# Kernel optimization log

Measured on AMD Instinct MI355X. Metric: run time of the kernel, lower is better.

Reference implementation:

```python
import jax, jax.numpy as jnp
import numpy as np

B, S, DM, H, D = 4, 2048, 1024, 16, 64
CAP = 15.0
EPS = 1e-6


def setup_inputs() -> dict:
    key = jax.random.key(0)
    ks = jax.random.split(key, 5)
    return {
        "x": jax.random.normal(ks[0], (B, S, DM), jnp.float32),
        "hidden_state": jnp.zeros((B, H, D, D), jnp.float32),
        "w_qkv": jax.random.normal(ks[1], (3 * H * D, DM), jnp.float32) * 0.02,
        "w_gate": jax.random.normal(ks[2], (3 * H, DM), jnp.float32) * 0.02,
        "w_out": jax.random.normal(ks[3], (DM, H * D), jnp.float32) * 0.02,
        "ln_w": jnp.ones((DM,), jnp.float32),
    }


def reference(x, hidden_state, w_qkv, w_gate, w_out, ln_w):
    Bq, Sq, DMq = x.shape
    residual = x
    # RMSNorm (computed in float32, matching the torch module)
    xf = x.astype(jnp.float32)
    var = jnp.mean(xf * xf, axis=-1, keepdims=True)
    xn = ln_w * (xf * jax.lax.rsqrt(var + EPS)).astype(x.dtype)
    # Fused qkv projection: (B,S,3,H,D)
    qkv = jnp.einsum('bsd,od->bso', xn, w_qkv).reshape(Bq, Sq, 3, H, D)
    q, k, v = qkv[:, :, 0], qkv[:, :, 1], qkv[:, :, 2]
    # Gates: (B,S,3,H) -> soft cap -> sigmoid
    gates = jnp.einsum('bsd,od->bso', xn, w_gate).reshape(Bq, Sq, 3, H)
    gates = jax.nn.sigmoid(CAP * jnp.tanh(gates / CAP))
    ig, fg, og = gates[:, :, 0], gates[:, :, 1], gates[:, :, 2]

    def step(h, inp):
        q_t, k_t, v_t, i_t, f_t, o_t = inp  # q/k/v: (B,H,D); gates: (B,H)
        kv = jnp.einsum('bhd,bhe->bhde', k_t, v_t)
        h = f_t[..., None, None] * h + i_t[..., None, None] * kv
        out = o_t[..., None] * jnp.einsum('bhd,bhde->bhe', q_t, h)
        return h, out

    xs = (q.swapaxes(0, 1), k.swapaxes(0, 1), v.swapaxes(0, 1),
          ig.swapaxes(0, 1), fg.swapaxes(0, 1), og.swapaxes(0, 1))
    h_final, outs = jax.lax.scan(step, hidden_state, xs)  # outs: (S,B,H,D)
    output = outs.swapaxes(0, 1).reshape(Bq, Sq, H * D)
    y = residual + output @ w_out.T
    return y, h_final
```

## Files before the change

kernel.cpp:

```cpp
#include <hip/hip_runtime.h>
#include <hip/hip_bf16.h>
#include <math.h>
#include <stdint.h>

#define Bq 4
#define Sq 2048
#define DMq 1024
#define Hq 16
#define Dq 64
#define CAPf 15.0f
#define EPSf 1e-6f
#define Tc 64
#define Cc (Sq / Tc)
#define QKVW (3 * Hq * Dq)
#define NGATE (3 * Hq)
#define NPAD 3200
#define MSc (Bq * Sq)

typedef __attribute__((ext_vector_type(8))) short short8;
typedef __attribute__((ext_vector_type(4))) float f32x4;
typedef __hip_bfloat16 bf16;

__device__ __forceinline__ float b2f(bf16 v) { return __bfloat162float(v); }
__device__ __forceinline__ bf16  f2b(float v) { return __float2bfloat16(v); }
__device__ __forceinline__ uint16_t f2bu(float f) {
    bf16 h = __float2bfloat16(f); uint16_t u; __builtin_memcpy(&u, &h, 2); return u;
}
__device__ __forceinline__ float bu2f(uint16_t u) {
    uint32_t x = ((uint32_t)u) << 16; float f; __builtin_memcpy(&f, &x, 4); return f;
}
__device__ __forceinline__ float gate_act(float v) {
    float t = v * (1.0f / CAPf);
    float e2 = __expf(2.0f * t);
    float th = 1.0f - 2.0f / (e2 + 1.0f);
    return 1.0f / (1.0f + __expf(-CAPf * th));
}

__global__ void prep_kernel(const float* __restrict__ x,
                            const float* __restrict__ ln_w,
                            const float* __restrict__ wqkv,
                            const float* __restrict__ wgate,
                            const float* __restrict__ wout,
                            bf16* __restrict__ xn,
                            bf16* __restrict__ wcomb, bf16* __restrict__ wob) {
    int tid = threadIdx.x;
    if (blockIdx.x < MSc) {
        int row = blockIdx.x;
        const float4* xr = (const float4*)(x + (size_t)row * DMq);
        float4 v = xr[tid];
        float ss = v.x*v.x + v.y*v.y + v.z*v.z + v.w*v.w;
        #pragma unroll
        for (int off = 32; off > 0; off >>= 1) ss += __shfl_down(ss, off);
        __shared__ float red[4];
        int lane = tid & 63, wv = tid >> 6;
        if (lane == 0) red[wv] = ss;
        __syncthreads();
        float tot = red[0] + red[1] + red[2] + red[3];
        float rs = rsqrtf(tot * (1.0f / DMq) + EPSf);
        float4 w4 = ((const float4*)ln_w)[tid];
        bf16 t[4] = {f2b(v.x * rs * w4.x), f2b(v.y * rs * w4.y),
                     f2b(v.z * rs * w4.z), f2b(v.w * rs * w4.w)};
        *(uint2*)(xn + (size_t)row * DMq + tid * 4) = *(uint2*)t;
        return;
    }
    const int n1 = QKVW * DMq / 4;
    const int n2 = (NPAD - QKVW) * DMq / 4;
    const int ng = NGATE * DMq / 4;
    const int n3 = DMq * Hq * Dq / 4;
    int i = (blockIdx.x - MSc) * 256 + tid;
    if (i < n1) {
        float4 v = ((const float4*)wqkv)[i];
        bf16 t[4] = {f2b(v.x), f2b(v.y), f2b(v.z), f2b(v.w)};
        ((uint2*)wcomb)[i] = *(uint2*)t;
    } else if (i < n1 + n2) {
        int j = i - n1;
        uint2 o = make_uint2(0u, 0u);
        if (j < ng) {
            float4 v = ((const float4*)wgate)[j];
            bf16 t[4] = {f2b(v.x), f2b(v.y), f2b(v.z), f2b(v.w)};
            o = *(uint2*)t;
        }
        ((uint2*)wcomb)[n1 + j] = o;
    } else if (i < n1 + n2 + n3) {
        int j = i - n1 - n2;
        float4 v = ((const float4*)wout)[j];
        bf16 t[4] = {f2b(v.x), f2b(v.y), f2b(v.z), f2b(v.w)};
        ((uint2*)wob)[j] = *(uint2*)t;
    }
}

enum Epi { EPI_BF16 = 0, EPI_GATE = 1, EPI_RESID = 2 };

template<int EPI>
__global__ __launch_bounds__(256) void gemm_mfma(const bf16* __restrict__ A,
                                                 const bf16* __restrict__ Bw,
                                                 const float* __restrict__ resid,
                                                 void* __restrict__ Cv,
                                                 int M, int N, int K) {
    __shared__ bf16 As[128 * 64];
    __shared__ bf16 Bs[128 * 64];
    const int tid = threadIdx.x;
    const int w = tid >> 6;
    const int l = tid & 63;
    const int wr = (w >> 1) * 64;
    const int wc = (w & 1) * 64;
    const int bm = blockIdx.y * 128;
    const int bn = blockIdx.x * 128;

    const int lrow = l >> 3;
    const int swzc = ((l & 7) ^ lrow) * 8;

    const int fl = l & 15;
    const int kb = l >> 4;
    const int rsw = l & 7;

    f32x4 acc[4][4];
    #pragma unroll
    for (int i = 0; i < 4; i++)
        #pragma unroll
        for (int j = 0; j < 4; j++) acc[i][j] = (f32x4){0.f, 0.f, 0.f, 0.f};

    for (int k0 = 0; k0 < K; k0 += 64) {
        __syncthreads();
        #pragma unroll
        for (int inst = 0; inst < 4; inst++) {
            int r0 = w * 32 + inst * 8;
            const bf16* gp = A + (size_t)(bm + r0 + lrow) * K + k0 + swzc;
            __builtin_amdgcn_global_load_lds(
                (const __attribute__((address_space(1))) uint32_t*)gp,
                (__attribute__((address_space(3))) uint32_t*)(As + r0 * 64),
                16, 0, 0);
        }
        #pragma unroll
        for (int inst = 0; inst < 4; inst++) {
            int r0 = w * 32 + inst * 8;
            if (bn + r0 < N) {
                const bf16* gp = Bw + (size_t)(bn + r0 + lrow) * K + k0 + swzc;
                __builtin_amdgcn_global_load_lds(
                    (const __attribute__((address_space(1))) uint32_t*)gp,
                    (__attribute__((address_space(3))) uint32_t*)(Bs + r0 * 64),
                    16, 0, 0);
            }
        }
        __syncthreads();
        #pragma unroll
        for (int kk2 = 0; kk2 < 2; kk2++) {
            const int koff = (((kk2 << 2) + kb) ^ rsw) * 8;
            short8 af[4], bfr[4];
            #pragma unroll
            for (int i = 0; i < 4; i++)
                af[i] = *(const short8*)(As + (wr + i * 16 + fl) * 64 + koff);
            #pragma unroll
            for (int j = 0; j < 4; j++)
                bfr[j] = *(const short8*)(Bs + (wc + j * 16 + fl) * 64 + koff);
            #pragma unroll
            for (int i = 0; i < 4; i++)
                #pragma unroll
                for (int j = 0; j < 4; j++)
                    acc[i][j] = __builtin_amdgcn_mfma_f32_16x16x32_bf16(
                        af[i], bfr[j], acc[i][j], 0, 0, 0);
        }
    }

    #pragma unroll
    for (int i = 0; i < 4; i++) {
        #pragma unroll
        for (int j = 0; j < 4; j++) {
            int col = bn + wc + j * 16 + fl;
            if (EPI == EPI_GATE && col >= N) continue;
            #pragma unroll
            for (int r = 0; r < 4; r++) {
                int row = bm + wr + i * 16 + kb * 4 + r;
                size_t idx = (size_t)row * N + col;
                float v = acc[i][j][r];
                if (EPI == EPI_GATE) {
                    ((float*)Cv)[idx] = gate_act(v);
                } else if (EPI == EPI_RESID) {
                    ((float*)Cv)[idx] = v + resid[idx];
                } else {
                    ((bf16*)Cv)[idx] = f2b(v);
                }
            }
        }
    }
}
template __global__ void gemm_mfma<EPI_BF16>(const bf16*, const bf16*, const float*, void*, int, int, int);
template __global__ void gemm_mfma<EPI_GATE>(const bf16*, const bf16*, const float*, void*, int, int, int);
template __global__ void gemm_mfma<EPI_RESID>(const bf16*, const bf16*, const float*, void*, int, int, int);

__global__ __launch_bounds__(64) void gemm_gates(const bf16* __restrict__ A,
                                                 const bf16* __restrict__ Bw,
                                                 float* __restrict__ gates_t,
                                                 int M, int K) {
    const int bm = blockIdx.x * 32;
    const int l = threadIdx.x, fl = l & 15, kb = l >> 4;
    f32x4 acc[2][3];
    #pragma unroll
    for (int i = 0; i < 2; i++)
        #pragma unroll
        for (int j = 0; j < 3; j++) acc[i][j] = (f32x4){0.f, 0.f, 0.f, 0.f};

    for (int ks = 0; ks < K; ks += 32) {
        short8 af[2], bf[3];
        #pragma unroll
        for (int i = 0; i < 2; i++)
            af[i] = *(const short8*)(A + (size_t)(bm + i * 16 + fl) * K + ks + kb * 8);
        #pragma unroll
        for (int j = 0; j < 3; j++)
            bf[j] = *(const short8*)(Bw + (size_t)(j * 16 + fl) * K + ks + kb * 8);
        #pragma unroll
        for (int i = 0; i < 2; i++)
            #pragma unroll
            for (int j = 0; j < 3; j++)
                acc[i][j] = __builtin_amdgcn_mfma_f32_16x16x32_bf16(af[i], bf[j], acc[i][j], 0, 0, 0);
    }
    #pragma unroll
    for (int i = 0; i < 2; i++)
        #pragma unroll
        for (int j = 0; j < 3; j++)
            #pragma unroll
            for (int r = 0; r < 4; r++) {
                int row = bm + i * 16 + kb * 4 + r;
                int g = j * 16 + fl;
                gates_t[(size_t)g * M + row] = gate_act(acc[i][j][r]);
            }
}

__global__ __launch_bounds__(64) void chunk_intra(const bf16* __restrict__ qkvb,
                                                  const float* __restrict__ gates,
                                                  bf16* __restrict__ attb,
                                                  bf16* __restrict__ LT,
                                                  float* __restrict__ oaArr,
                                                  float* __restrict__ Fch) {
    const int blk = blockIdx.x;
    const int c  = blk & (Cc - 1);
    const int bh = blk >> 5;
    const int b = bh >> 4, hh = bh & 15;
    const int l = threadIdx.x;
    const int s0 = c * Tc;

    __shared__ bf16 KTs[4096];
    __shared__ bf16 VTs[4096];
    __shared__ float rowS[64], pcolS[64], wstS[64];

    const int rix = b * Sq + s0 + l;
    float ig = gates[(size_t)(0 * Hq + hh) * MSc + rix];
    float fg = gates[(size_t)(1 * Hq + hh) * MSc + rix];
    float og = gates[(size_t)(2 * Hq + hh) * MSc + rix];
    float la = __logf(fg);
    #pragma unroll
    for (int off = 1; off < 64; off <<= 1) {
        float v = __shfl_up(la, off);
        if (l >= off) la += v;
    }
    float la63 = __shfl(la, 63);
    float li = __logf(ig);
    rowS[l]  = la + __logf(og);
    pcolS[l] = li - la;
    wstS[l]  = __expf(la63 - la + li);
    float oa = og * __expf(la);
    oaArr[(size_t)blk * 64 + l] = oa;
    if (l == 0) Fch[blk] = __expf(la63);
    __syncthreads();

    const int cg = l & 7, rp = l >> 3;
    const size_t rowBase = (size_t)(b * Sq + s0);
    const int kcol = (Hq + hh) * Dq, vcol = (2 * Hq + hh) * Dq;
    #pragma unroll
    for (int pass = 0; pass < 4; pass++) {
        int j0 = pass * 16 + rp * 2;
        const bf16* r0 = qkvb + (rowBase + j0) * QKVW;
        const bf16* r1 = qkvb + (rowBase + j0 + 1) * QKVW;
        short8 k0 = *(const short8*)(r0 + kcol + cg * 8);
        short8 k1 = *(const short8*)(r1 + kcol + cg * 8);
        short8 v0 = *(const short8*)(r0 + vcol + cg * 8);
        short8 v1 = *(const short8*)(r1 + vcol + cg * 8);
        float w0 = wstS[j0], w1 = wstS[j0 + 1];
        #pragma unroll
        for (int s = 0; s < 8; s++) {
            int cc = cg * 8 + s;
            int base = cc * 64 + ((((j0 >> 3) ^ (cc & 7) ^ (cc >> 3))) << 3) + (j0 & 7);
            uint32_t kp = (uint32_t)f2bu(bu2f((uint16_t)k0[s]) * w0)
                        | ((uint32_t)f2bu(bu2f((uint16_t)k1[s]) * w1) << 16);
            uint32_t vp = (uint32_t)(uint16_t)v0[s] | ((uint32_t)(uint16_t)v1[s] << 16);
            *(uint32_t*)&KTs[base] = kp;
            *(uint32_t*)&VTs[base] = vp;
        }
    }
    __syncthreads();

    const int fl = l & 15, kb = l >> 4;

    f32x4 accL[4][4];
    #pragma unroll
    for (int i = 0; i < 4; i++)
        #pragma unroll
        for (int j = 0; j < 4; j++) accL[i][j] = (f32x4){0.f, 0.f, 0.f, 0.f};
    #pragma unroll
    for (int ks = 0; ks < 2; ks++) {
        short8 vt[4], kt[4];
        #pragma unroll
        for (int i = 0; i < 4; i++) {
            int row = i * 16 + fl;
            int koff = (((ks * 4 + kb) ^ (row & 7) ^ (row >> 3))) << 3;
            vt[i] = *(const short8*)(VTs + row * 64 + koff);
            kt[i] = *(const short8*)(KTs + row * 64 + koff);
        }
        #pragma unroll
        for (int i = 0; i < 4; i++)
            #pragma unroll
            for (int j = 0; j < 4; j++)
                accL[i][j] = __builtin_amdgcn_mfma_f32_16x16x32_bf16(vt[i], kt[j], accL[i][j], 0, 0, 0);
    }
    #pragma unroll
    for (int i = 0; i < 4; i++)
        #pragma unroll
        for (int j = 0; j < 4; j++)
            #pragma unroll
            for (int r = 0; r < 4; r++) {
                int rr = i * 16 + kb * 4 + r, cc2 = j * 16 + fl;
                LT[(size_t)blk * 4096 + rr * 64 + cc2] = f2b(accL[i][j][r]);
            }

    const bf16* Qb = qkvb + rowBase * QKVW + hh * Dq;
    const bf16* Kb = qkvb + rowBase * QKVW + kcol;
    f32x4 accS[4][4];
    #pragma unroll
    for (int i = 0; i < 4; i++)
        #pragma unroll
        for (int j = 0; j < 4; j++) accS[i][j] = (f32x4){0.f, 0.f, 0.f, 0.f};
    #pragma unroll
    for (int ks = 0; ks < 2; ks++) {
        short8 qf[4], kf[4];
        #pragma unroll
        for (int i = 0; i < 4; i++)
            qf[i] = *(const short8*)(Qb + (size_t)(i * 16 + fl) * QKVW + ks * 32 + kb * 8);
        #pragma unroll
        for (int j = 0; j < 4; j++)
            kf[j] = *(const short8*)(Kb + (size_t)(j * 16 + fl) * QKVW + ks * 32 + kb * 8);
        #pragma unroll
        for (int i = 0; i < 4; i++)
            #pragma unroll
            for (int j = 0; j < 4; j++)
                accS[i][j] = __builtin_amdgcn_mfma_f32_16x16x32_bf16(qf[i], kf[j], accS[i][j], 0, 0, 0);
    }

    __syncthreads();
    bf16* Ps = KTs;
    #pragma unroll
    for (int i = 0; i < 4; i++) {
        #pragma unroll
        for (int j = 0; j < 4; j++) {
            int jj = j * 16 + fl;
            float pc = pcolS[jj];
            #pragma unroll
            for (int r = 0; r < 4; r++) {
                int t = i * 16 + kb * 4 + r;
                float p = (jj <= t) ? __expf(rowS[t] + pc) * accS[i][j][r] : 0.f;
                int slot = (jj >> 3) ^ (t & 7) ^ (t >> 3);
                Ps[t * 64 + slot * 8 + (jj & 7)] = f2b(p);
            }
        }
    }
    __syncthreads();

    f32x4 accO[4][4];
    #pragma unroll
    for (int i = 0; i < 4; i++)
        #pragma unroll
        for (int j = 0; j < 4; j++) accO[i][j] = (f32x4){0.f, 0.f, 0.f, 0.f};
    #pragma unroll
    for (int ks = 0; ks < 2; ks++) {
        short8 pf[4], vt[4];
        #pragma unroll
        for (int i = 0; i < 4; i++) {
            int row = i * 16 + fl;
            int koff = (((ks * 4 + kb) ^ (row & 7) ^ (row >> 3))) << 3;
            pf[i] = *(const short8*)(Ps  + row * 64 + koff);
            vt[i] = *(const short8*)(VTs + row * 64 + koff);
        }
        #pragma unroll
        for (int i = 0; i < 4; i++)
            #pragma unroll
            for (int j = 0; j < 4; j++)
                accO[i][j] = __builtin_amdgcn_mfma_f32_16x16x32_bf16(pf[i], vt[j], accO[i][j], 0, 0, 0);
    }

    #pragma unroll
    for (int i = 0; i < 4; i++)
        #pragma unroll
        for (int j = 0; j < 4; j++)
            #pragma unroll
            for (int r = 0; r < 4; r++) {
                int rr = i * 16 + kb * 4 + r, cc2 = j * 16 + fl;
                attb[(rowBase + rr) * (Hq * Dq) + hh * Dq + cc2] = f2b(accO[i][j][r]);
            }
}

__global__ __launch_bounds__(256) void scan_pass2(bf16* __restrict__ LH,
                                                  const float* __restrict__ Fchunk,
                                                  const float* __restrict__ h0,
                                                  float* __restrict__ hfin) {
    int idx = blockIdx.x * 256 + threadIdx.x;
    int bh = idx >> 12;
    int ed = idx & 4095;
    int e = ed >> 6, d = ed & 63;
    float run = h0[(size_t)bh * 4096 + d * 64 + e];
    #pragma unroll
    for (int c = 0; c < Cc; c++) {
        float Fv = Fchunk[bh * Cc + c];
        size_t off = ((size_t)bh * Cc + c) * 4096 + ed;
        float Lv = b2f(LH[off]);
        LH[off] = f2b(run);
        run = Fv * run + Lv;
    }
    hfin[(size_t)bh * 4096 + d * 64 + e] = run;
}

__global__ __launch_bounds__(64) void chunk_cross(const bf16* __restrict__ qkvb,
                                                  const bf16* __restrict__ HT,
                                                  const float* __restrict__ oaArr,
                                                  bf16* __restrict__ attb) {
    const int blk = blockIdx.x;
    const int c = blk & (Cc - 1);
    const int bh = blk >> 5;
    const int b = bh >> 4, hh = bh & 15;
    const int l = threadIdx.x, fl = l & 15, kb = l >> 4;
    const size_t rowBase = (size_t)(b * Sq + c * Tc);
    __shared__ float oaS[64];
    oaS[l] = oaArr[(size_t)blk * 64 + l];
    __syncthreads();
    const bf16* Qb = qkvb + rowBase * QKVW + hh * Dq;
    const bf16* Hb = HT + (size_t)blk * 4096;
    f32x4 acc[4][4];
    #pragma unroll
    for (int i = 0; i < 4; i++)
        #pragma unroll
        for (int j = 0; j < 4; j++) acc[i][j] = (f32x4){0.f, 0.f, 0.f, 0.f};
    #pragma unroll
    for (int ks = 0; ks < 2; ks++) {
        short8 qf[4], hf[4];
        #pragma unroll
        for (int i = 0; i < 4; i++)
            qf[i] = *(const short8*)(Qb + (size_t)(i * 16 + fl) * QKVW + ks * 32 + kb * 8);
        #pragma unroll
        for (int j = 0; j < 4; j++)
            hf[j] = *(const short8*)(Hb + (j * 16 + fl) * 64 + ks * 32 + kb * 8);
        #pragma unroll
        for (int i = 0; i < 4; i++)
            #pragma unroll
            for (int j = 0; j < 4; j++)
                acc[i][j] = __builtin_amdgcn_mfma_f32_16x16x32_bf16(qf[i], hf[j], acc[i][j], 0, 0, 0);
    }
    #pragma unroll
    for (int i = 0; i < 4; i++)
        #pragma unroll
        for (int j = 0; j < 4; j++)
            #pragma unroll
            for (int r = 0; r < 4; r++) {
                int t = i * 16 + kb * 4 + r, e = j * 16 + fl;
                size_t idx = (rowBase + t) * (Hq * Dq) + hh * Dq + e;
                attb[idx] = f2b(b2f(attb[idx]) + oaS[t] * acc[i][j][r]);
            }
}

extern "C" void kernel_launch(void* const* d_in, const int* in_sizes, int n_in,
                              void* d_out, int out_size, void* d_ws, size_t ws_size,
                              hipStream_t stream) {
    const float* x      = (const float*)d_in[0];
    const float* h0     = (const float*)d_in[1];
    const float* w_qkv  = (const float*)d_in[2];
    const float* w_gate = (const float*)d_in[3];
    const float* w_out  = (const float*)d_in[4];
    const float* ln_w   = (const float*)d_in[5];

    const size_t MS = (size_t)Bq * Sq;
    const size_t BH = (size_t)Bq * Hq;

    float* p = (float*)d_ws;
    bf16*  xnb   = (bf16*)p;  p += MS * DMq / 2;
    bf16*  qkvb  = (bf16*)p;  p += MS * QKVW / 2;
    float* gates = p;         p += MS * NGATE;
    float* oaArr = p;         p += BH * Cc * Tc;
    float* Fch   = p;         p += BH * Cc;
    bf16*  LT    = (bf16*)p;  p += BH * Cc * Dq * Dq / 2;
    bf16*  wcomb = (bf16*)p;  p += (size_t)NPAD * DMq / 2;
    bf16*  wob   = (bf16*)p;  p += (size_t)DMq * Hq * Dq / 2;
    size_t need = (size_t)(p - (float*)d_ws) * sizeof(float);
    if (ws_size < need) return;
    bf16* attb = xnb;

    float* y    = (float*)d_out;
    float* hfin = y + MS * DMq;

    const int cvt_n = (QKVW * DMq + (NPAD - QKVW) * DMq + DMq * Hq * Dq) / 4;
    const int cvt_blocks = (cvt_n + 255) / 256;
    prep_kernel<<<dim3(MS + cvt_blocks), dim3(256), 0, stream>>>(
        x, ln_w, w_qkv, w_gate, w_out, xnb, wcomb, wob);

    gemm_mfma<EPI_BF16><<<dim3(QKVW / 128, MS / 128), dim3(256), 0, stream>>>(
        xnb, wcomb, nullptr, qkvb, (int)MS, QKVW, DMq);

    gemm_gates<<<dim3(MS / 32), dim3(64), 0, stream>>>(
        xnb, wcomb + (size_t)QKVW * DMq, gates, (int)MS, DMq);

    chunk_intra<<<dim3(BH * Cc), dim3(64), 0, stream>>>(qkvb, gates, attb, LT, oaArr, Fch);
    scan_pass2<<<dim3(BH * 4096 / 256), dim3(256), 0, stream>>>(LT, Fch, h0, hfin);
    chunk_cross<<<dim3(BH * Cc), dim3(64), 0, stream>>>(qkvb, LT, oaArr, attb);

    gemm_mfma<EPI_RESID><<<dim3(DMq / 128, MS / 128), dim3(256), 0, stream>>>(
        attb, wob, x, y, (int)MS, DMq, Hq * Dq);
}
```

Before: 160.5 us.

## Replace QKV GEMM with 256x256 tile, 8-wave, double-buffered direct-to-LDS pipeline

Adds a new QKV projection kernel using 256x256 output tiles, 512 threads, and global_load_lds direct-to-shared loads into a double-buffered, XOR-swizzled LDS layout. Global loads for the next K tiles are interleaved between MFMA phases with explicit barriers, vmcnt waits and priority hints. The aim is to raise arithmetic intensity and hide memory latency compared with the old 128x128 kernel. In exchange it uses 128KB of LDS and many accumulator registers, which limits occupancy, and the grid shrinks to 12x32 blocks, which may underfill the CUs.

```diff
diff --git a/kernel.cpp b/kernel.cpp
--- a/kernel.cpp
+++ b/kernel.cpp
@@ -35,6 +35,9 @@
     float th = 1.0f - 2.0f / (e2 + 1.0f);
     return 1.0f / (1.0f + __expf(-CAPf * th));
 }
+
+#define BARR do { __builtin_amdgcn_s_barrier(); __builtin_amdgcn_sched_barrier(0); } while (0)
+#define VM6  asm volatile("s_waitcnt vmcnt(6)" ::: "memory")
 
 __global__ void prep_kernel(const float* __restrict__ x,
                             const float* __restrict__ ln_w,
@@ -89,6 +92,130 @@
     }
 }
 
+__global__ __launch_bounds__(512, 2) void gemm_qkv8(const bf16* __restrict__ A,
+                                                    const bf16* __restrict__ Bw,
+                                                    bf16* __restrict__ Cb,
+                                                    int M, int N, int K) {
+    __shared__ bf16 As[2 * 256 * 64];
+    __shared__ bf16 Bs[2 * 256 * 64];
+    const int tid = threadIdx.x;
+    const int w = tid >> 6;
+    const int l = tid & 63;
+    const int wm = w >> 2;
+    const int wn = w & 3;
+    const int bm = blockIdx.y * 256;
+    const int bn = blockIdx.x * 256;
+    const int lrow = l >> 3;
+    const int swzc = ((l & 7) ^ lrow) * 8;
+    const int fl = l & 15;
+    const int kb = l >> 4;
+    const int rsw = l & 7;
+    const int nt = K >> 6;
+    const int niter = K >> 7;
+
+    f32x4 acc[8][4];
+    #pragma unroll
+    for (int i = 0; i < 8; i++)
+        #pragma unroll
+        for (int j = 0; j < 4; j++) acc[i][j] = (f32x4){0.f, 0.f, 0.f, 0.f};
+
+    auto stageA = [&](int d, int h, int li, int kt) {
+        int k0 = (kt < nt ? kt : nt - 1) << 6;
+        int r0 = h * 128 + li * 64 + w * 8;
+        const bf16* gp = A + (size_t)(bm + r0 + lrow) * K + k0 + swzc;
+        __builtin_amdgcn_global_load_lds(
+            (const __attribute__((address_space(1))) uint32_t*)gp,
+            (__attribute__((address_space(3))) uint32_t*)(As + d * 16384 + r0 * 64), 16, 0, 0);
+    };
+    auto stageB = [&](int d, int h, int li, int kt) {
+        int k0 = (kt < nt ? kt : nt - 1) << 6;
+        int r0 = h * 128 + li * 64 + w * 8;
+        const bf16* gp = Bw + (size_t)(bn + r0 + lrow) * K + k0 + swzc;
+        __builtin_amdgcn_global_load_lds(
+            (const __attribute__((address_space(1))) uint32_t*)gp,
+            (__attribute__((address_space(3))) uint32_t*)(Bs + d * 16384 + r0 * 64), 16, 0, 0);
+    };
+    auto ldsA = [&](int d, int q, short8 (&af)[2][2]) {
+        #pragma unroll
+        for (int ii = 0; ii < 2; ii++)
+            #pragma unroll
+            for (int kk = 0; kk < 2; kk++) {
+                int R = wm * 128 + q * 32 + ii * 16 + fl;
+                af[ii][kk] = *(const short8*)(As + d * 16384 + R * 64 + (((kk << 2) + kb) ^ rsw) * 8);
+            }
+    };
+    auto ldsB = [&](int d, short8 (&bfr)[4][2]) {
+        #pragma unroll
+        for (int j = 0; j < 4; j++)
+            #pragma unroll
+            for (int kk = 0; kk < 2; kk++) {
+                int R = wn * 64 + j * 16 + fl;
+                bfr[j][kk] = *(const short8*)(Bs + d * 16384 + R * 64 + (((kk << 2) + kb) ^ rsw) * 8);
+            }
+    };
+    auto mm = [&](int q, short8 (&af)[2][2], short8 (&bfr)[4][2]) {
+        __builtin_amdgcn_s_setprio(1);
+        #pragma unroll
+        for (int ii = 0; ii < 2; ii++)
+            #pragma unroll
+            for (int j = 0; j < 4; j++)
+                #pragma unroll
+                for (int kk = 0; kk < 2; kk++)
+                    acc[q * 2 + ii][j] = __builtin_amdgcn_mfma_f32_16x16x32_bf16(
+                        af[ii][kk], bfr[j][kk], acc[q * 2 + ii][j], 0, 0, 0);
+        __builtin_amdgcn_s_setprio(0);
+    };
+
+    stageB(0, 0, 0, 0); stageB(0, 0, 1, 0); stageB(0, 1, 0, 0); stageB(0, 1, 1, 0);
+    stageA(0, 0, 0, 0); stageA(0, 1, 0, 0); stageA(0, 0, 1, 0); stageA(0, 1, 1, 0);
+    stageB(1, 0, 0, 1); stageB(1, 0, 1, 1); stageB(1, 1, 0, 1); stageB(1, 1, 1, 1);
+    stageA(1, 0, 0, 1); stageA(1, 1, 0, 1);
+    VM6; BARR;
+
+    short8 bfr[4][2], af[2][2];
+    #pragma unroll 1
+    for (int i = 0; i < niter; i++) {
+        const int t1 = 2 * i + 1, n0 = 2 * i + 2, n1 = 2 * i + 3;
+        ldsB(0, bfr); ldsA(0, 0, af);
+        stageA(1, 0, 1, t1); stageA(1, 1, 1, t1);
+        BARR; mm(0, af, bfr); BARR;
+        ldsA(0, 1, af);
+        stageB(0, 0, 0, n0); stageB(0, 0, 1, n0);
+        BARR; mm(1, af, bfr); BARR;
+        ldsA(0, 2, af);
+        stageB(0, 1, 0, n0); stageB(0, 1, 1, n0);
+        BARR; mm(2, af, bfr); BARR;
+        ldsA(0, 3, af);
+        stageA(0, 0, 0, n0); stageA(0, 1, 0, n0);
+        VM6; BARR; mm(3, af, bfr); BARR;
+        ldsB(1, bfr); ldsA(1, 0, af);
+        stageA(0, 0, 1, n0); stageA(0, 1, 1, n0);
+        BARR; mm(0, af, bfr); BARR;
+        ldsA(1, 1, af);
+        stageB(1, 0, 0, n1); stageB(1, 0, 1, n1);
+        BARR; mm(1, af, bfr); BARR;
+        ldsA(1, 2, af);
+        stageB(1, 1, 0, n1); stageB(1, 1, 1, n1);
+        BARR; mm(2, af, bfr); BARR;
+        ldsA(1, 3, af);
+        stageA(1, 0, 0, n1); stageA(1, 1, 0, n1);
+        VM6; BARR; mm(3, af, bfr); BARR;
+    }
+    asm volatile("s_waitcnt vmcnt(0)" ::: "memory");
+
+    #pragma unroll
+    for (int fi = 0; fi < 8; fi++)
+        #pragma unroll
+        for (int j = 0; j < 4; j++) {
+            int col = bn + wn * 64 + j * 16 + fl;
+            #pragma unroll
+            for (int r = 0; r < 4; r++) {
+                int row = bm + wm * 128 + fi * 16 + kb * 4 + r;
+                Cb[(size_t)row * N + col] = f2b(acc[fi][j][r]);
+            }
+        }
+}
+
 enum Epi { EPI_BF16 = 0, EPI_GATE = 1, EPI_RESID = 2 };
 
 template<int EPI>
@@ -498,8 +625,8 @@
     prep_kernel<<<dim3(MS + cvt_blocks), dim3(256), 0, stream>>>(
         x, ln_w, w_qkv, w_gate, w_out, xnb, wcomb, wob);
 
-    gemm_mfma<EPI_BF16><<<dim3(QKVW / 128, MS / 128), dim3(256), 0, stream>>>(
-        xnb, wcomb, nullptr, qkvb, (int)MS, QKVW, DMq);
+    gemm_qkv8<<<dim3(QKVW / 256, MS / 256), dim3(512), 0, stream>>>(
+        xnb, wcomb, qkvb, (int)MS, QKVW, DMq);
 
     gemm_gates<<<dim3(MS / 32), dim3(64), 0, stream>>>(
         xnb, wcomb + (size_t)QKVW * DMq, gates, (int)MS, DMq);
```

Result: slower. 167.5 us (+4.4%).
